# Kernel tuning notes

Measured on AMD Instinct MI355X. Metric: run time of the kernel, lower is better.

## Reference

```python
import jax, jax.numpy as jnp
import numpy as np

# Faithful JAX port of the approxmatch EMD kernel (Fan et al.) wrapped by emdDist.
# 10 soft-assignment (auction-style) iterations with annealed temperature level=-4^j,
# j = 7..-1, final iteration level = 0. match is accumulated transport mass;
# cost[b] = sum_{k,l} match[b,k,l] * ||x1_k - x2_l||.

_EPS = 1e-9


def _approxmatch(xyz1, xyz2):
    # xyz1: (b, n, 3), xyz2: (b, m, 3)
    b, n, _ = xyz1.shape
    m = xyz2.shape[1]
    factorl = max(n, m) / n
    factorr = max(n, m) / m
    remainL = jnp.full((b, n), factorl, dtype=xyz1.dtype)   # mass left on xyz1 points
    remainR = jnp.full((b, m), factorr, dtype=xyz1.dtype)   # capacity left on xyz2 points
    # pairwise squared distances (b, n, m)
    d2 = jnp.sum((xyz1[:, :, None, :] - xyz2[:, None, :, :]) ** 2, axis=-1)
    match = jnp.zeros((b, n, m), dtype=xyz1.dtype)
    for j in range(7, -3, -1):  # j = 7, 6, ..., -1, -2
        level = 0.0 if j == -2 else -(4.0 ** j)
        # proposal weights from each left point, scaled by remaining right capacity
        w = jnp.exp(level * d2) * remainR[:, None, :]                      # (b,n,m)
        w = w / (jnp.sum(w, axis=-1, keepdims=True) + _EPS) * remainL[:, :, None]
        # right points accept at most their remaining capacity
        sumr = jnp.sum(w, axis=1) + _EPS                                   # (b,m)
        ratio = jnp.minimum(remainR / sumr, 1.0)                           # (b,m)
        delta = w * ratio[:, None, :]                                      # accepted transfer
        match = match + delta
        remainL = jnp.maximum(remainL - jnp.sum(delta, axis=-1), 0.0)
        remainR = jnp.maximum(remainR - jnp.sum(delta, axis=1), 0.0)
    return match, d2


def setup_inputs() -> dict:
    key = jax.random.key(0)
    k1, k2 = jax.random.split(key)
    B, N, M = 8, 4096, 4096
    input1 = jax.random.normal(k1, (B, N, 3), dtype=jnp.float32)
    input2 = jax.random.normal(k2, (B, M, 3), dtype=jnp.float32)
    return {"input1": input1, "input2": input2}


def reference(input1, input2):
    match, d2 = _approxmatch(input1, input2)
    # original CUDA backward treats match as a constant -> stop_gradient
    match = jax.lax.stop_gradient(match)
    dist = jnp.sqrt(jnp.maximum(d2, 1e-12))
    cost = jnp.sum(match * dist, axis=(1, 2))  # (b,)
    return cost
```

## Files before the change

### kernel.cpp

```cpp
#include <hip/hip_runtime.h>

#define NPTS 4096
#define NB   8
#define TPB  256
#define MBLK 4
#define EPSC 1e-9f

#define EXP2(x)  __builtin_amdgcn_exp2f(x)
#define RCPF(x)  __builtin_amdgcn_rcpf(x)
#define SQRTF(x) __builtin_amdgcn_sqrtf(x)

__global__ __launch_bounds__(TPB) void sort_kernel(
    const float* __restrict__ x1, const float* __restrict__ x2,
    float4* __restrict__ x1p, float4* __restrict__ x2p,
    float4* __restrict__ bb8)
{
  __shared__ unsigned int   hist[4096];
  __shared__ unsigned short codes[4096];
  __shared__ unsigned int   part[TPB];

  const int set = blockIdx.x, b = blockIdx.y;
  const float* src = set ? x2 : x1;
  float4* dst = set ? x2p : x1p;
  const int tid = threadIdx.x;

  for (int i = tid; i < 4096; i += TPB) hist[i] = 0;
  __syncthreads();

  for (int j = 0; j < NPTS / TPB; ++j) {
    int n = j * TPB + tid;
    const float* p = src + ((size_t)b * NPTS + n) * 3;
    int qx = min(max((int)((p[0] + 4.f) * 2.f), 0), 15);
    int qy = min(max((int)((p[1] + 4.f) * 2.f), 0), 15);
    int qz = min(max((int)((p[2] + 4.f) * 2.f), 0), 15);
    auto ex = [](int v) {
      return (v & 1) | ((v & 2) << 2) | ((v & 4) << 4) | ((v & 8) << 6);
    };
    int code = ex(qx) | (ex(qy) << 1) | (ex(qz) << 2);
    codes[n] = (unsigned short)code;
    atomicAdd(&hist[code], 1u);
  }
  __syncthreads();

  unsigned int loc[16], s = 0;
#pragma unroll
  for (int j = 0; j < 16; ++j) { loc[j] = s; s += hist[tid * 16 + j]; }
  part[tid] = s;
  __syncthreads();
  if (tid == 0) {
    unsigned int run = 0;
    for (int t = 0; t < TPB; ++t) { unsigned int v = part[t]; part[t] = run; run += v; }
  }
  __syncthreads();
  {
    unsigned int base = part[tid];
#pragma unroll
    for (int j = 0; j < 16; ++j) hist[tid * 16 + j] = base + loc[j];
  }
  __syncthreads();

  for (int j = 0; j < NPTS / TPB; ++j) {
    int n = j * TPB + tid;
    const float* p = src + ((size_t)b * NPTS + n) * 3;
    unsigned int pos = atomicAdd(&hist[codes[n]], 1u);
    dst[(size_t)b * NPTS + pos] = make_float4(p[0], p[1], p[2], 0.f);
  }
  __syncthreads();

  for (int g = tid; g < 512; g += TPB) {
    float mnx = 1e30f, mny = 1e30f, mnz = 1e30f;
    float mxx = -1e30f, mxy = -1e30f, mxz = -1e30f;
#pragma unroll
    for (int j = 0; j < 8; ++j) {
      float4 p = dst[(size_t)b * NPTS + g * 8 + j];
      mnx = fminf(mnx, p.x); mxx = fmaxf(mxx, p.x);
      mny = fminf(mny, p.y); mxy = fmaxf(mxy, p.y);
      mnz = fminf(mnz, p.z); mxz = fmaxf(mxz, p.z);
    }
    size_t bi = ((size_t)(set * NB + b) * 512 + g) * 2;
    bb8[bi + 0] = make_float4(mnx, mny, mnz, 0.f);
    bb8[bi + 1] = make_float4(mxx, mxy, mxz, 0.f);
  }
}

template<int MODE, bool SUBCULL, int CHUNK>
__global__ __launch_bounds__(TPB) void ca_kernel(
    const float4* __restrict__ x2p, const float4* __restrict__ x1p,
    const float2* __restrict__ urbuf,
    float* __restrict__ dbufP, float* __restrict__ rsumP,
    const float4* __restrict__ bb8s,
    float* __restrict__ out, float sc)
{
  __shared__ float4 x2s[CHUNK];
  __shared__ float2 urs[CHUNK];

  const int tid = threadIdx.x;
  const int nchunk = blockIdx.x, mseg = blockIdx.y, b = blockIdx.z;

  if (MODE == 0 && nchunk == 0 && mseg == 0 && tid == 0) out[b] = 0.f;

  for (int mm = tid; mm < CHUNK; mm += TPB) {
    int m = mseg * CHUNK + mm;
    float4 q = x2p[(size_t)b * NPTS + m];
    float sx = sc * q.x, sy = sc * q.y, sz = sc * q.z;
    float nq = fmaf(sz, sz, fmaf(sy, sy, sx * sx));
    x2s[mm] = make_float4(-2.f * sx, -2.f * sy, -2.f * sz, nq);
    urs[mm] = (MODE == 0) ? make_float2(0.f, 1.f) : urbuf[(size_t)b * NPTS + m];
  }
  __syncthreads();

  const int n0 = nchunk * (TPB * MBLK) + tid * MBLK;
  float px[MBLK], py[MBLK], pz[MBLK], np[MBLK], dacc[MBLK], racc[MBLK];
#pragma unroll
  for (int k = 0; k < MBLK; ++k) {
    float4 p = x1p[(size_t)b * NPTS + n0 + k];
    px[k] = sc * p.x; py[k] = sc * p.y; pz[k] = sc * p.z;
    np[k] = fmaf(pz[k], pz[k], fmaf(py[k], py[k], px[k] * px[k]));
    dacc[k] = 0.f; racc[k] = 0.f;
  }

  float rrsum = 0.f;
  if (MODE == 2) {
    float v = 0.f;
    for (int l = (tid & 63); l < CHUNK; l += 64) v += urs[l].y;
#pragma unroll
    for (int off = 1; off < 64; off <<= 1) v += __shfl_xor(v, off);
    rrsum = v;
  }

  auto proc = [&](int mm) {
    float4 q = x2s[mm];
    float2 ur = urs[mm];
    float ds2[MBLK];
#pragma unroll
    for (int k = 0; k < MBLK; ++k)
      ds2[k] = fmaf(q.x, px[k], fmaf(q.y, py[k], fmaf(q.z, pz[k], np[k] + q.w)));
    if (MODE == 2) {
#pragma unroll
      for (int k = 0; k < MBLK; ++k)
        racc[k] = fmaf(EXP2(-ds2[k]), ur.x, racc[k]);
    } else {
#pragma unroll
      for (int k = 0; k < MBLK; ++k) {
        float en = EXP2(-ds2[k]);
        dacc[k] = fmaf(en, ur.y, dacc[k]);
        if (MODE == 1) { float e2 = en * en; racc[k] = fmaf(e2 * e2, ur.x, racc[k]); }
      }
    }
  };

  if (SUBCULL) {
    float mnx = fminf(fminf(px[0], px[1]), fminf(px[2], px[3]));
    float mny = fminf(fminf(py[0], py[1]), fminf(py[2], py[3]));
    float mnz = fminf(fminf(pz[0], pz[1]), fminf(pz[2], pz[3]));
    float mxx = fmaxf(fmaxf(px[0], px[1]), fmaxf(px[2], px[3]));
    float mxy = fmaxf(fmaxf(py[0], py[1]), fmaxf(py[2], py[3]));
    float mxz = fmaxf(fmaxf(pz[0], pz[1]), fmaxf(pz[2], pz[3]));
#pragma unroll
    for (int off = 1; off < 64; off <<= 1) {
      mnx = fminf(mnx, __shfl_xor(mnx, off));
      mny = fminf(mny, __shfl_xor(mny, off));
      mnz = fminf(mnz, __shfl_xor(mnz, off));
      mxx = fmaxf(mxx, __shfl_xor(mxx, off));
      mxy = fmaxf(mxy, __shfl_xor(mxy, off));
      mxz = fmaxf(mxz, __shfl_xor(mxz, off));
    }
    constexpr int NSUB = CHUNK / 8;
    const int lane = tid & 63;
    bool go = false;
    if (lane < NSUB) {
      size_t bi = ((size_t)b * 512 + mseg * NSUB + lane) * 2;
      float4 smin = bb8s[bi], smax = bb8s[bi + 1];
      float gx = fmaxf(0.f, fmaxf(sc * smin.x - mxx, mnx - sc * smax.x));
      float gy = fmaxf(0.f, fmaxf(sc * smin.y - mxy, mny - sc * smax.y));
      float gz = fmaxf(0.f, fmaxf(sc * smin.z - mxz, mnz - sc * smax.z));
      go = fmaf(gx, gx, fmaf(gy, gy, gz * gz)) < 126.f;
    }
    unsigned long long mask = __ballot(go);
    for (int s = 0; s < NSUB; ++s) {
      if (!((mask >> s) & 1)) continue;
#pragma unroll
      for (int j = 0; j < 8; ++j) proc(s * 8 + j);
    }
  } else {
#pragma unroll 4
    for (int mm = 0; mm < CHUNK; ++mm) proc(mm);
  }

  size_t base = ((size_t)mseg * NB + b) * NPTS + n0;
  if (MODE == 2) {
#pragma unroll
    for (int k = 0; k < MBLK; ++k) dacc[k] = rrsum;
  }
  *(float4*)&dbufP[base] = make_float4(dacc[0], dacc[1], dacc[2], dacc[3]);
  if (MODE >= 1)
    *(float4*)&rsumP[base] = make_float4(racc[0], racc[1], racc[2], racc[3]);
}

template<int LVL0, bool SUBCULL, int CHUNK>
__global__ __launch_bounds__(TPB) void b_kernel(
    const float4* __restrict__ x1p, const float* __restrict__ abuf,
    const float4* __restrict__ x2p,
    float* __restrict__ s0P, float* __restrict__ s1P,
    const float4* __restrict__ bb8s, float sc, float inv_s)
{
  __shared__ float4 x1s[CHUNK];
  __shared__ float  as_[CHUNK];

  const int tid = threadIdx.x;
  const int mchunk = blockIdx.x, nsegi = blockIdx.y, b = blockIdx.z;

  for (int nn = tid; nn < CHUNK; nn += TPB) {
    int n = nsegi * CHUNK + nn;
    float4 p = x1p[(size_t)b * NPTS + n];
    float sx = sc * p.x, sy = sc * p.y, sz = sc * p.z;
    float npv = fmaf(sz, sz, fmaf(sy, sy, sx * sx));
    x1s[nn] = make_float4(-2.f * sx, -2.f * sy, -2.f * sz, npv);
    as_[nn] = abuf[(size_t)b * NPTS + n];
  }
  __syncthreads();

  const int m0 = mchunk * (TPB * MBLK) + tid * MBLK;
  float qx[MBLK], qy[MBLK], qz[MBLK], nq[MBLK], s0a[MBLK], s1a[MBLK];
#pragma unroll
  for (int k = 0; k < MBLK; ++k) {
    float4 q = x2p[(size_t)b * NPTS + m0 + k];
    qx[k] = sc * q.x; qy[k] = sc * q.y; qz[k] = sc * q.z;
    nq[k] = fmaf(qz[k], qz[k], fmaf(qy[k], qy[k], qx[k] * qx[k]));
    s0a[k] = 0.f; s1a[k] = 0.f;
  }

  float asum = 0.f;
  if (LVL0) {
    float v = 0.f;
    for (int l = (tid & 63); l < CHUNK; l += 64) v += as_[l];
#pragma unroll
    for (int off = 1; off < 64; off <<= 1) v += __shfl_xor(v, off);
    asum = v;
  }

  auto proc = [&](int nn) {
    float4 p = x1s[nn];
    float av = as_[nn];
    float ds2[MBLK];
#pragma unroll
    for (int k = 0; k < MBLK; ++k)
      ds2[k] = fmaf(p.x, qx[k], fmaf(p.y, qy[k], fmaf(p.z, qz[k], nq[k] + p.w)));
    if (LVL0) {
#pragma unroll
      for (int k = 0; k < MBLK; ++k)
        s1a[k] = fmaf(av, SQRTF(__builtin_fabsf(ds2[k])), s1a[k]);
    } else {
#pragma unroll
      for (int k = 0; k < MBLK; ++k) {
        float tt = av * EXP2(-ds2[k]);
        s0a[k] += tt;
        s1a[k] = fmaf(tt, SQRTF(__builtin_fabsf(ds2[k])), s1a[k]);
      }
    }
  };

  if (SUBCULL) {
    float mnx = fminf(fminf(qx[0], qx[1]), fminf(qx[2], qx[3]));
    float mny = fminf(fminf(qy[0], qy[1]), fminf(qy[2], qy[3]));
    float mnz = fminf(fminf(qz[0], qz[1]), fminf(qz[2], qz[3]));
    float mxx = fmaxf(fmaxf(qx[0], qx[1]), fmaxf(qx[2], qx[3]));
    float mxy = fmaxf(fmaxf(qy[0], qy[1]), fmaxf(qy[2], qy[3]));
    float mxz = fmaxf(fmaxf(qz[0], qz[1]), fmaxf(qz[2], qz[3]));
#pragma unroll
    for (int off = 1; off < 64; off <<= 1) {
      mnx = fminf(mnx, __shfl_xor(mnx, off));
      mny = fminf(mny, __shfl_xor(mny, off));
      mnz = fminf(mnz, __shfl_xor(mnz, off));
      mxx = fmaxf(mxx, __shfl_xor(mxx, off));
      mxy = fmaxf(mxy, __shfl_xor(mxy, off));
      mxz = fmaxf(mxz, __shfl_xor(mxz, off));
    }
    constexpr int NSUB = CHUNK / 8;
    const int lane = tid & 63;
    bool go = false;
    if (lane < NSUB) {
      size_t bi = ((size_t)b * 512 + nsegi * NSUB + lane) * 2;
      float4 smin = bb8s[bi], smax = bb8s[bi + 1];
      float gx = fmaxf(0.f, fmaxf(sc * smin.x - mxx, mnx - sc * smax.x));
      float gy = fmaxf(0.f, fmaxf(sc * smin.y - mxy, mny - sc * smax.y));
      float gz = fmaxf(0.f, fmaxf(sc * smin.z - mxz, mnz - sc * smax.z));
      go = fmaf(gx, gx, fmaf(gy, gy, gz * gz)) < 126.f;
    }
    unsigned long long mask = __ballot(go);
    for (int s = 0; s < NSUB; ++s) {
      if (!((mask >> s) & 1)) continue;
#pragma unroll
      for (int j = 0; j < 8; ++j) proc(s * 8 + j);
    }
  } else {
#pragma unroll 4
    for (int nn = 0; nn < CHUNK; ++nn) proc(nn);
  }

  size_t base = ((size_t)nsegi * NB + b) * NPTS + m0;
  if (LVL0) {
#pragma unroll
    for (int k = 0; k < MBLK; ++k) s0a[k] = asum;
  }
  *(float4*)&s0P[base] = make_float4(s0a[0], s0a[1], s0a[2], s0a[3]);
  *(float4*)&s1P[base] = make_float4(s1a[0] * inv_s, s1a[1] * inv_s,
                                     s1a[2] * inv_s, s1a[3] * inv_s);
}

template<int NSEG>
__global__ __launch_bounds__(256) void r1_kernel(
    const float* __restrict__ dbufP, const float* __restrict__ rsumP,
    float* __restrict__ lbuf, float* __restrict__ dtot,
    float* __restrict__ abuf, int iter)
{
  constexpr int SL = 8, EPB = 32, PPS = NSEG / SL;
  __shared__ float redD[SL][EPB];
  __shared__ float redR[SL][EPB];

  const int e  = threadIdx.x & (EPB - 1);
  const int sl = threadIdx.x / EPB;
  const int idx = blockIdx.x * EPB + e;
  const size_t plane = (size_t)NB * NPTS;

  float ad = 0.f, ar = 0.f;
#pragma unroll
  for (int s = 0; s < PPS; ++s)
    ad += dbufP[(size_t)(sl * PPS + s) * plane + idx];
  if (iter > 0) {
#pragma unroll
    for (int s = 0; s < PPS; ++s)
      ar += rsumP[(size_t)(sl * PPS + s) * plane + idx];
  }
  redD[sl][e] = ad;
  redR[sl][e] = ar;
  __syncthreads();

  if (sl == 0) {
    float dnew = 0.f, rs = 0.f;
#pragma unroll
    for (int s = 0; s < SL; ++s) { dnew += redD[s][e]; rs += redR[s][e]; }
    float rl = 1.f;
    if (iter > 0) {
      float rlp = lbuf[idx];
      float ap  = rlp * RCPF(dtot[idx] + EPSC);
      rl = fmaxf(rlp - ap * rs, 0.f);
    }
    lbuf[idx] = rl;
    dtot[idx] = dnew;
    abuf[idx] = rl * RCPF(dnew + EPSC);
  }
}

template<int NSEG, bool LAST>
__global__ __launch_bounds__(256) void r2_kernel(
    const float* __restrict__ s0P, const float* __restrict__ s1P,
    float2* __restrict__ urbuf, float* __restrict__ out, int iter)
{
  constexpr int SL = 8, EPB = 32, PPS = NSEG / SL;
  __shared__ float redA[SL][EPB];
  __shared__ float redB[SL][EPB];

  const int e  = threadIdx.x & (EPB - 1);
  const int sl = threadIdx.x / EPB;
  const int idx = blockIdx.x * EPB + e;
  const int b = idx >> 12;
  const size_t plane = (size_t)NB * NPTS;

  float a0 = 0.f, a1 = 0.f;
#pragma unroll
  for (int s = 0; s < PPS; ++s) {
    a0 += s0P[(size_t)(sl * PPS + s) * plane + idx];
    a1 += s1P[(size_t)(sl * PPS + s) * plane + idx];
  }
  redA[sl][e] = a0;
  redB[sl][e] = a1;
  __syncthreads();

  float cpart = 0.f;
  if (sl == 0) {
    float s0 = 0.f, s1 = 0.f;
#pragma unroll
    for (int s = 0; s < SL; ++s) { s0 += redA[s][e]; s1 += redB[s][e]; }
    float rr    = (iter == 0) ? 1.f : urbuf[idx].y;
    float sumr  = fmaf(rr, s0, EPSC);
    float ratio = fminf(rr * RCPF(sumr), 1.f);
    float u     = rr * ratio;
    if (!LAST) urbuf[idx] = make_float2(u, fmaxf(rr - u * s0, 0.f));
    cpart = u * s1;
  }
  __syncthreads();
  if (sl == 0) redA[0][e] = cpart;
  __syncthreads();
  if (threadIdx.x == 0) {
    float acc = 0.f;
#pragma unroll
    for (int j = 0; j < EPB; ++j) acc += redA[0][j];
    atomicAdd(out + b, acc);
  }
}

template<int NSEG>
static void run_all(const float* x1, const float* x2, float* out, float* ws,
                    hipStream_t stream)
{
  constexpr int CHUNK = NPTS / NSEG;
  const size_t plane = (size_t)NB * NPTS;

  float*  bufA = ws;
  float*  bufB = bufA + (size_t)NSEG * plane;
  float4* x1p  = (float4*)(bufB + (size_t)NSEG * plane);
  float4* x2p  = x1p + plane;
  float*  dtot = (float*)(x2p + plane);
  float*  lbuf = dtot + plane;
  float*  abuf = lbuf + plane;
  float2* urbuf = (float2*)(abuf + plane);
  float4* bb8  = (float4*)(urbuf + plane);
  float4* bb8_1 = bb8;
  float4* bb8_2 = bb8 + (size_t)NB * 512 * 2;

  const double L2E = 1.4426950408889634074;
  const double lv[10] = {-16384.0, -4096.0, -1024.0, -256.0, -64.0,
                         -16.0, -4.0, -1.0, -0.25, 0.0};
  float scl[10], inv_s[10];
  for (int i = 0; i < 10; ++i) {
    double c2 = lv[i] * L2E;
    scl[i]   = (i == 9) ? 1.f : (float)sqrt(-c2);
    inv_s[i] = (i == 9) ? 1.f : (float)(1.0 / sqrt(-c2));
  }

  dim3 gmain(NPTS / (TPB * MBLK), NSEG, NB), bmain(TPB);
  dim3 gr(NB * NPTS / 32), br(256);

  sort_kernel<<<dim3(2, NB), bmain, 0, stream>>>(x1, x2, x1p, x2p, bb8);

  ca_kernel<0, true, CHUNK><<<gmain, bmain, 0, stream>>>(
      x2p, x1p, urbuf, bufA, bufB, bb8_2, out, scl[0]);

  for (int i = 0; i < 10; ++i) {
    r1_kernel<NSEG><<<gr, br, 0, stream>>>(bufA, bufB, lbuf, dtot, abuf, i);

    if (i <= 6)
      b_kernel<0, true, CHUNK><<<gmain, bmain, 0, stream>>>(
          x1p, abuf, x2p, bufA, bufB, bb8_1, scl[i], inv_s[i]);
    else if (i <= 8)
      b_kernel<0, false, CHUNK><<<gmain, bmain, 0, stream>>>(
          x1p, abuf, x2p, bufA, bufB, bb8_1, scl[i], inv_s[i]);
    else
      b_kernel<1, false, CHUNK><<<gmain, bmain, 0, stream>>>(
          x1p, abuf, x2p, bufA, bufB, bb8_1, 1.f, 1.f);

    if (i < 9)
      r2_kernel<NSEG, false><<<gr, br, 0, stream>>>(bufA, bufB, urbuf, out, i);
    else
      r2_kernel<NSEG, true><<<gr, br, 0, stream>>>(bufA, bufB, urbuf, out, i);

    if (i <= 5)
      ca_kernel<1, true, CHUNK><<<gmain, bmain, 0, stream>>>(
          x2p, x1p, urbuf, bufA, bufB, bb8_2, out, scl[i + 1]);
    else if (i <= 7)
      ca_kernel<1, false, CHUNK><<<gmain, bmain, 0, stream>>>(
          x2p, x1p, urbuf, bufA, bufB, bb8_2, out, scl[i + 1]);
    else if (i == 8)
      ca_kernel<2, false, CHUNK><<<gmain, bmain, 0, stream>>>(
          x2p, x1p, urbuf, bufA, bufB, bb8_2, out, scl[8]);
  }
}

extern "C" void kernel_launch(void* const* d_in, const int* in_sizes, int n_in,
                              void* d_out, int out_size, void* d_ws, size_t ws_size,
                              hipStream_t stream) {
  const float* x1 = (const float*)d_in[0];
  const float* x2 = (const float*)d_in[1];
  float* out = (float*)d_out;
  float* ws  = (float*)d_ws;

  const size_t plane = (size_t)NB * NPTS;
  auto need = [&](int nseg) {
    return (size_t)(2 * nseg + 13) * plane * sizeof(float)
         + (size_t)2 * NB * 512 * 2 * sizeof(float4);
  };

  if (ws_size >= need(64))      run_all<64>(x1, x2, out, ws, stream);
  else if (ws_size >= need(32)) run_all<32>(x1, x2, out, ws, stream);
  else                          run_all<16>(x1, x2, out, ws, stream);
}
```

Measured before the change: 983.6 us.

## Replace bounding-box subchunk culling with per-pair exp skipping and 8-point register blocking

Removes the precomputed 8-point bounding boxes and the wave-level ballot culling. Each thread now holds 8 points instead of 4 and, at high temperature levels, skips the exp and accumulation for a partner point when all 8 scaled distances exceed the underflow threshold. The skip is enabled for fewer iterations than before, and the segment count drops from 64 to 32. Doubling the register block halves the grid and raises register pressure. The per-thread branch can diverge within a wave, and the early iterations now evaluate distances for every pair where whole subchunks used to be culled.

```diff
diff --git a/kernel.cpp b/kernel.cpp
--- a/kernel.cpp
+++ b/kernel.cpp
@@ -3,7 +3,7 @@
 #define NPTS 4096
 #define NB   8
 #define TPB  256
-#define MBLK 4
+#define MBLK 8
 #define EPSC 1e-9f
 
 #define EXP2(x)  __builtin_amdgcn_exp2f(x)
@@ -12,8 +12,7 @@
 
 __global__ __launch_bounds__(TPB) void sort_kernel(
     const float* __restrict__ x1, const float* __restrict__ x2,
-    float4* __restrict__ x1p, float4* __restrict__ x2p,
-    float4* __restrict__ bb8)
+    float4* __restrict__ x1p, float4* __restrict__ x2p)
 {
   __shared__ unsigned int   hist[4096];
   __shared__ unsigned short codes[4096];
@@ -65,30 +64,13 @@
     unsigned int pos = atomicAdd(&hist[codes[n]], 1u);
     dst[(size_t)b * NPTS + pos] = make_float4(p[0], p[1], p[2], 0.f);
   }
-  __syncthreads();
-
-  for (int g = tid; g < 512; g += TPB) {
-    float mnx = 1e30f, mny = 1e30f, mnz = 1e30f;
-    float mxx = -1e30f, mxy = -1e30f, mxz = -1e30f;
-#pragma unroll
-    for (int j = 0; j < 8; ++j) {
-      float4 p = dst[(size_t)b * NPTS + g * 8 + j];
-      mnx = fminf(mnx, p.x); mxx = fmaxf(mxx, p.x);
-      mny = fminf(mny, p.y); mxy = fmaxf(mxy, p.y);
-      mnz = fminf(mnz, p.z); mxz = fmaxf(mxz, p.z);
-    }
-    size_t bi = ((size_t)(set * NB + b) * 512 + g) * 2;
-    bb8[bi + 0] = make_float4(mnx, mny, mnz, 0.f);
-    bb8[bi + 1] = make_float4(mxx, mxy, mxz, 0.f);
-  }
-}
-
-template<int MODE, bool SUBCULL, int CHUNK>
+}
+
+template<int MODE, bool PSKIP, int CHUNK>
 __global__ __launch_bounds__(TPB) void ca_kernel(
     const float4* __restrict__ x2p, const float4* __restrict__ x1p,
     const float2* __restrict__ urbuf,
     float* __restrict__ dbufP, float* __restrict__ rsumP,
-    const float4* __restrict__ bb8s,
     float* __restrict__ out, float sc)
 {
   __shared__ float4 x2s[CHUNK];
@@ -128,7 +110,8 @@
     rrsum = v;
   }
 
-  auto proc = [&](int mm) {
+#pragma unroll 2
+  for (int mm = 0; mm < CHUNK; ++mm) {
     float4 q = x2s[mm];
     float2 ur = urs[mm];
     float ds2[MBLK];
@@ -140,51 +123,21 @@
       for (int k = 0; k < MBLK; ++k)
         racc[k] = fmaf(EXP2(-ds2[k]), ur.x, racc[k]);
     } else {
-#pragma unroll
-      for (int k = 0; k < MBLK; ++k) {
-        float en = EXP2(-ds2[k]);
-        dacc[k] = fmaf(en, ur.y, dacc[k]);
-        if (MODE == 1) { float e2 = en * en; racc[k] = fmaf(e2 * e2, ur.x, racc[k]); }
+      bool go = true;
+      if (PSKIP) {
+        float dmin = fminf(fminf(fminf(ds2[0], ds2[1]), fminf(ds2[2], ds2[3])),
+                           fminf(fminf(ds2[4], ds2[5]), fminf(ds2[6], ds2[7])));
+        go = dmin < 126.f;
+      }
+      if (go) {
+#pragma unroll
+        for (int k = 0; k < MBLK; ++k) {
+          float en = EXP2(-ds2[k]);
+          dacc[k] = fmaf(en, ur.y, dacc[k]);
+          if (MODE == 1) { float e2 = en * en; racc[k] = fmaf(e2 * e2, ur.x, racc[k]); }
+        }
       }
     }
-  };
-
-  if (SUBCULL) {
-    float mnx = fminf(fminf(px[0], px[1]), fminf(px[2], px[3]));
-    float mny = fminf(fminf(py[0], py[1]), fminf(py[2], py[3]));
-    float mnz = fminf(fminf(pz[0], pz[1]), fminf(pz[2], pz[3]));
-    float mxx = fmaxf(fmaxf(px[0], px[1]), fmaxf(px[2], px[3]));
-    float mxy = fmaxf(fmaxf(py[0], py[1]), fmaxf(py[2], py[3]));
-    float mxz = fmaxf(fmaxf(pz[0], pz[1]), fmaxf(pz[2], pz[3]));
-#pragma unroll
-    for (int off = 1; off < 64; off <<= 1) {
-      mnx = fminf(mnx, __shfl_xor(mnx, off));
-      mny = fminf(mny, __shfl_xor(mny, off));
-      mnz = fminf(mnz, __shfl_xor(mnz, off));
-      mxx = fmaxf(mxx, __shfl_xor(mxx, off));
-      mxy = fmaxf(mxy, __shfl_xor(mxy, off));
-      mxz = fmaxf(mxz, __shfl_xor(mxz, off));
-    }
-    constexpr int NSUB = CHUNK / 8;
-    const int lane = tid & 63;
-    bool go = false;
-    if (lane < NSUB) {
-      size_t bi = ((size_t)b * 512 + mseg * NSUB + lane) * 2;
-      float4 smin = bb8s[bi], smax = bb8s[bi + 1];
-      float gx = fmaxf(0.f, fmaxf(sc * smin.x - mxx, mnx - sc * smax.x));
-      float gy = fmaxf(0.f, fmaxf(sc * smin.y - mxy, mny - sc * smax.y));
-      float gz = fmaxf(0.f, fmaxf(sc * smin.z - mxz, mnz - sc * smax.z));
-      go = fmaf(gx, gx, fmaf(gy, gy, gz * gz)) < 126.f;
-    }
-    unsigned long long mask = __ballot(go);
-    for (int s = 0; s < NSUB; ++s) {
-      if (!((mask >> s) & 1)) continue;
-#pragma unroll
-      for (int j = 0; j < 8; ++j) proc(s * 8 + j);
-    }
-  } else {
-#pragma unroll 4
-    for (int mm = 0; mm < CHUNK; ++mm) proc(mm);
   }
 
   size_t base = ((size_t)mseg * NB + b) * NPTS + n0;
@@ -192,17 +145,20 @@
 #pragma unroll
     for (int k = 0; k < MBLK; ++k) dacc[k] = rrsum;
   }
-  *(float4*)&dbufP[base] = make_float4(dacc[0], dacc[1], dacc[2], dacc[3]);
-  if (MODE >= 1)
-    *(float4*)&rsumP[base] = make_float4(racc[0], racc[1], racc[2], racc[3]);
-}
-
-template<int LVL0, bool SUBCULL, int CHUNK>
+  *(float4*)&dbufP[base]     = make_float4(dacc[0], dacc[1], dacc[2], dacc[3]);
+  *(float4*)&dbufP[base + 4] = make_float4(dacc[4], dacc[5], dacc[6], dacc[7]);
+  if (MODE >= 1) {
+    *(float4*)&rsumP[base]     = make_float4(racc[0], racc[1], racc[2], racc[3]);
+    *(float4*)&rsumP[base + 4] = make_float4(racc[4], racc[5], racc[6], racc[7]);
+  }
+}
+
+template<int LVL0, bool PSKIP, int CHUNK>
 __global__ __launch_bounds__(TPB) void b_kernel(
     const float4* __restrict__ x1p, const float* __restrict__ abuf,
     const float4* __restrict__ x2p,
     float* __restrict__ s0P, float* __restrict__ s1P,
-    const float4* __restrict__ bb8s, float sc, float inv_s)
+    float sc, float inv_s)
 {
   __shared__ float4 x1s[CHUNK];
   __shared__ float  as_[CHUNK];
@@ -239,7 +195,8 @@
     asum = v;
   }
 
-  auto proc = [&](int nn) {
+#pragma unroll 2
+  for (int nn = 0; nn < CHUNK; ++nn) {
     float4 p = x1s[nn];
     float av = as_[nn];
     float ds2[MBLK];
@@ -251,51 +208,21 @@
       for (int k = 0; k < MBLK; ++k)
         s1a[k] = fmaf(av, SQRTF(__builtin_fabsf(ds2[k])), s1a[k]);
     } else {
-#pragma unroll
-      for (int k = 0; k < MBLK; ++k) {
-        float tt = av * EXP2(-ds2[k]);
-        s0a[k] += tt;
-        s1a[k] = fmaf(tt, SQRTF(__builtin_fabsf(ds2[k])), s1a[k]);
+      bool go = true;
+      if (PSKIP) {
+        float dmin = fminf(fminf(fminf(ds2[0], ds2[1]), fminf(ds2[2], ds2[3])),
+                           fminf(fminf(ds2[4], ds2[5]), fminf(ds2[6], ds2[7])));
+        go = dmin < 126.f;
+      }
+      if (go) {
+#pragma unroll
+        for (int k = 0; k < MBLK; ++k) {
+          float tt = av * EXP2(-ds2[k]);
+          s0a[k] += tt;
+          s1a[k] = fmaf(tt, SQRTF(__builtin_fabsf(ds2[k])), s1a[k]);
+        }
       }
     }
-  };
-
-  if (SUBCULL) {
-    float mnx = fminf(fminf(qx[0], qx[1]), fminf(qx[2], qx[3]));
-    float mny = fminf(fminf(qy[0], qy[1]), fminf(qy[2], qy[3]));
-    float mnz = fminf(fminf(qz[0], qz[1]), fminf(qz[2], qz[3]));
-    float mxx = fmaxf(fmaxf(qx[0], qx[1]), fmaxf(qx[2], qx[3]));
-    float mxy = fmaxf(fmaxf(qy[0], qy[1]), fmaxf(qy[2], qy[3]));
-    float mxz = fmaxf(fmaxf(qz[0], qz[1]), fmaxf(qz[2], qz[3]));
-#pragma unroll
-    for (int off = 1; off < 64; off <<= 1) {
-      mnx = fminf(mnx, __shfl_xor(mnx, off));
-      mny = fminf(mny, __shfl_xor(mny, off));
-      mnz = fminf(mnz, __shfl_xor(mnz, off));
-      mxx = fmaxf(mxx, __shfl_xor(mxx, off));
-      mxy = fmaxf(mxy, __shfl_xor(mxy, off));
-      mxz = fmaxf(mxz, __shfl_xor(mxz, off));
-    }
-    constexpr int NSUB = CHUNK / 8;
-    const int lane = tid & 63;
-    bool go = false;
-    if (lane < NSUB) {
-      size_t bi = ((size_t)b * 512 + nsegi * NSUB + lane) * 2;
-      float4 smin = bb8s[bi], smax = bb8s[bi + 1];
-      float gx = fmaxf(0.f, fmaxf(sc * smin.x - mxx, mnx - sc * smax.x));
-      float gy = fmaxf(0.f, fmaxf(sc * smin.y - mxy, mny - sc * smax.y));
-      float gz = fmaxf(0.f, fmaxf(sc * smin.z - mxz, mnz - sc * smax.z));
-      go = fmaf(gx, gx, fmaf(gy, gy, gz * gz)) < 126.f;
-    }
-    unsigned long long mask = __ballot(go);
-    for (int s = 0; s < NSUB; ++s) {
-      if (!((mask >> s) & 1)) continue;
-#pragma unroll
-      for (int j = 0; j < 8; ++j) proc(s * 8 + j);
-    }
-  } else {
-#pragma unroll 4
-    for (int nn = 0; nn < CHUNK; ++nn) proc(nn);
   }
 
   size_t base = ((size_t)nsegi * NB + b) * NPTS + m0;
@@ -303,9 +230,12 @@
 #pragma unroll
     for (int k = 0; k < MBLK; ++k) s0a[k] = asum;
   }
-  *(float4*)&s0P[base] = make_float4(s0a[0], s0a[1], s0a[2], s0a[3]);
-  *(float4*)&s1P[base] = make_float4(s1a[0] * inv_s, s1a[1] * inv_s,
-                                     s1a[2] * inv_s, s1a[3] * inv_s);
+  *(float4*)&s0P[base]     = make_float4(s0a[0], s0a[1], s0a[2], s0a[3]);
+  *(float4*)&s0P[base + 4] = make_float4(s0a[4], s0a[5], s0a[6], s0a[7]);
+  *(float4*)&s1P[base]     = make_float4(s1a[0] * inv_s, s1a[1] * inv_s,
+                                         s1a[2] * inv_s, s1a[3] * inv_s);
+  *(float4*)&s1P[base + 4] = make_float4(s1a[4] * inv_s, s1a[5] * inv_s,
+                                         s1a[6] * inv_s, s1a[7] * inv_s);
 }
 
 template<int NSEG>
@@ -415,9 +345,6 @@
   float*  lbuf = dtot + plane;
   float*  abuf = lbuf + plane;
   float2* urbuf = (float2*)(abuf + plane);
-  float4* bb8  = (float4*)(urbuf + plane);
-  float4* bb8_1 = bb8;
-  float4* bb8_2 = bb8 + (size_t)NB * 512 * 2;
 
   const double L2E = 1.4426950408889634074;
   const double lv[10] = {-16384.0, -4096.0, -1024.0, -256.0, -64.0,
@@ -432,38 +359,38 @@
   dim3 gmain(NPTS / (TPB * MBLK), NSEG, NB), bmain(TPB);
   dim3 gr(NB * NPTS / 32), br(256);
 
-  sort_kernel<<<dim3(2, NB), bmain, 0, stream>>>(x1, x2, x1p, x2p, bb8);
+  sort_kernel<<<dim3(2, NB), bmain, 0, stream>>>(x1, x2, x1p, x2p);
 
   ca_kernel<0, true, CHUNK><<<gmain, bmain, 0, stream>>>(
-      x2p, x1p, urbuf, bufA, bufB, bb8_2, out, scl[0]);
+      x2p, x1p, urbuf, bufA, bufB, out, scl[0]);
 
   for (int i = 0; i < 10; ++i) {
     r1_kernel<NSEG><<<gr, br, 0, stream>>>(bufA, bufB, lbuf, dtot, abuf, i);
 
-    if (i <= 6)
+    if (i <= 2)
       b_kernel<0, true, CHUNK><<<gmain, bmain, 0, stream>>>(
-          x1p, abuf, x2p, bufA, bufB, bb8_1, scl[i], inv_s[i]);
+          x1p, abuf, x2p, bufA, bufB, scl[i], inv_s[i]);
     else if (i <= 8)
       b_kernel<0, false, CHUNK><<<gmain, bmain, 0, stream>>>(
-          x1p, abuf, x2p, bufA, bufB, bb8_1, scl[i], inv_s[i]);
+          x1p, abuf, x2p, bufA, bufB, scl[i], inv_s[i]);
     else
       b_kernel<1, false, CHUNK><<<gmain, bmain, 0, stream>>>(
-          x1p, abuf, x2p, bufA, bufB, bb8_1, 1.f, 1.f);
+          x1p, abuf, x2p, bufA, bufB, 1.f, 1.f);
 
     if (i < 9)
       r2_kernel<NSEG, false><<<gr, br, 0, stream>>>(bufA, bufB, urbuf, out, i);
     else
       r2_kernel<NSEG, true><<<gr, br, 0, stream>>>(bufA, bufB, urbuf, out, i);
 
-    if (i <= 5)
+    if (i <= 1)
       ca_kernel<1, true, CHUNK><<<gmain, bmain, 0, stream>>>(
-          x2p, x1p, urbuf, bufA, bufB, bb8_2, out, scl[i + 1]);
+          x2p, x1p, urbuf, bufA, bufB, out, scl[i + 1]);
     else if (i <= 7)
       ca_kernel<1, false, CHUNK><<<gmain, bmain, 0, stream>>>(
-          x2p, x1p, urbuf, bufA, bufB, bb8_2, out, scl[i + 1]);
+          x2p, x1p, urbuf, bufA, bufB, out, scl[i + 1]);
     else if (i == 8)
       ca_kernel<2, false, CHUNK><<<gmain, bmain, 0, stream>>>(
-          x2p, x1p, urbuf, bufA, bufB, bb8_2, out, scl[8]);
+          x2p, x1p, urbuf, bufA, bufB, out, scl[8]);
   }
 }
 
@@ -477,11 +404,9 @@
 
   const size_t plane = (size_t)NB * NPTS;
   auto need = [&](int nseg) {
-    return (size_t)(2 * nseg + 13) * plane * sizeof(float)
-         + (size_t)2 * NB * 512 * 2 * sizeof(float4);
+    return (size_t)(2 * nseg + 13) * plane * sizeof(float);
   };
 
-  if (ws_size >= need(64))      run_all<64>(x1, x2, out, ws, stream);
-  else if (ws_size >= need(32)) run_all<32>(x1, x2, out, ws, stream);
+  if (ws_size >= need(32))      run_all<32>(x1, x2, out, ws, stream);
   else                          run_all<16>(x1, x2, out, ws, stream);
 }
```

Result: no change. 979.6 us (-0.4%).
